# Optimization experiments

Measured on AMD Instinct MI355X. Metric: run time of the kernel, lower is better.

## Reference

```python
import jax, jax.numpy as jnp
import numpy as np

NUM_HEADS = 8
SCALE = 1.0
BN_EPS = 1e-5


def _mlp1d(x, W1, g1, b1, W2):
    # Conv1d(k=1, bias=False) -> BatchNorm1d (training-mode batch stats) -> ReLU -> Conv1d(k=1, bias=False)
    h = jnp.einsum('oi,bil->bol', W1, x)
    mu = h.mean(axis=(0, 2), keepdims=True)
    var = h.var(axis=(0, 2), keepdims=True)  # biased var, as torch BN training
    h = (h - mu) * jax.lax.rsqrt(var + BN_EPS)
    h = jax.nn.relu(h * g1[None, :, None] + b1[None, :, None])
    return jnp.einsum('oi,bil->bol', W2, h)


def setup_inputs() -> dict:
    key = jax.random.key(0)
    ks = jax.random.split(key, 8)
    b, c, hh, ww = 64, 2048, 14, 14
    hid, out = 4096, 256
    d = {'x': jax.random.normal(ks[0], (b, c, hh, ww), jnp.float32)}

    def w(k, o, i):
        return jax.random.normal(k, (o, i), jnp.float32) * np.float32(1.0 / np.sqrt(i))

    i = 1
    for pre in ('p', 'pp', 'po'):  # proj, proj_pixel, proj_obj
        d[pre + 'W1'] = w(ks[i], hid, c); i += 1
        d[pre + 'G1'] = jnp.ones((hid,), jnp.float32)
        d[pre + 'B1'] = jnp.zeros((hid,), jnp.float32)
        d[pre + 'W2'] = w(ks[i], out, hid); i += 1
    return d


def reference(x, pW1, pG1, pB1, pW2, ppW1, ppG1, ppB1, ppW2, poW1, poG1, poB1, poW2):
    b, c, h, w = x.shape
    xf = x.reshape(b, c, h * w)                      # flatten(2)
    x_pool = xf.mean(axis=2, keepdims=True)          # adaptive_avg_pool2d(x, 1)
    z_g = _mlp1d(x_pool, pW1, pG1, pB1, pW2)         # [b, 256, 1]
    z_feat = _mlp1d(xf, ppW1, ppG1, ppB1, ppW2)      # [b, 256, hw]
    # F.normalize(dim=1) with eps=1e-12, then /scale
    nrm = jnp.maximum(jnp.linalg.norm(z_feat, axis=1, keepdims=True), 1e-12)
    attn = (z_feat / nrm) / SCALE
    attn = attn.reshape(b, NUM_HEADS, -1, h * w)     # [b, nh, 256/nh, hw]
    attn = jax.nn.softmax(attn, axis=-1)
    x4 = xf.reshape(b, NUM_HEADS, c // NUM_HEADS, h * w)
    # torch.matmul(x, obj_attn.transpose(3, 2)) : [b,nh,c/nh,hw] @ [b,nh,hw,q]
    obj_val = jnp.einsum('bnkl,bnql->bnkq', x4, attn).reshape(b, c, -1)  # [b, c, 256/nh]
    obj_val = _mlp1d(obj_val, poW1, poG1, poB1, poW2)                    # [b, 256, 32]
    return z_g, obj_val
```

## Files before the change

kernel.cpp:

```cpp
#include <hip/hip_runtime.h>
#include <hip/hip_bf16.h>

using bf16 = __hip_bfloat16;
typedef __bf16 bf16x8v __attribute__((ext_vector_type(8)));
typedef float f32x4 __attribute__((ext_vector_type(4)));

#define BN_EPS 1e-5f

__device__ __forceinline__ float ldval(const float* p) { return *p; }
__device__ __forceinline__ float ldval(const bf16* p)  { return __bfloat162float(*p); }
__device__ __forceinline__ void stval(float* p, float v) { *p = v; }
__device__ __forceinline__ void stval(bf16* p, float v)  { *p = __float2bfloat16(v); }

__device__ __forceinline__ void gload_lds16(const void* g, void* l) {
    __builtin_amdgcn_global_load_lds(
        (const __attribute__((address_space(1))) unsigned int*)g,
        (__attribute__((address_space(3))) unsigned int*)l,
        16, 0, 0);
}

template<typename TC>
__global__ __launch_bounds__(512, 2) void mfma_tn8(
    const bf16* __restrict__ A, const bf16* __restrict__ B, TC* __restrict__ C,
    int M, int N, int K, float* __restrict__ ps, float* __restrict__ pq)
{
    __shared__ char lds[131072];
    const int NT = K >> 6;
    const int tid = threadIdx.x;
    const int lane = tid & 63;
    const int wv = tid >> 6;
    const int wm = wv >> 2;
    const int wn = wv & 3;

    const int nbx = gridDim.x;
    int flat = blockIdx.y * nbx + blockIdx.x;
    const int cpx = (nbx * gridDim.y) >> 3;
    flat = (flat & 7) * cpx + (flat >> 3);
    const int mtile = flat / nbx;
    const long m0 = (long)mtile * 256;
    const long n0 = (long)(flat % nbx) * 256;

    const int trow = tid >> 3;
    const int ks = (((tid & 7) ^ ((tid >> 3) & 7)) << 3);
    const bf16* Arow0 = A + (m0 + trow) * (long)K + ks;
    const bf16* Brow0 = B + (n0 + trow) * (long)K + ks;
    char* ldsA = (char*)lds + tid * 16;
    char* ldsB = (char*)lds + 32768 + tid * 16;

    auto stage_a = [&](int bbuf, int kt) {
        const bf16* g = Arow0 + ((long)kt << 6);
        char* d = ldsA + (bbuf << 16);
        gload_lds16(g, d);
        gload_lds16(g + ((long)K << 6),  d + 8192);
        gload_lds16(g + ((long)K << 7),  d + 16384);
        gload_lds16(g + 192L * (long)K,  d + 24576);
    };
    auto stage_b = [&](int bbuf, int kt) {
        const bf16* g = Brow0 + ((long)kt << 6);
        char* d = ldsB + (bbuf << 16);
        gload_lds16(g, d);
        gload_lds16(g + ((long)K << 6),  d + 8192);
        gload_lds16(g + ((long)K << 7),  d + 16384);
        gload_lds16(g + 192L * (long)K,  d + 24576);
    };

    const int fr = lane & 15, fc = lane >> 4;
    const int ca0 = ((fc ^ (fr & 7)) << 4);
    const int ca1 = (((4 + fc) ^ (fr & 7)) << 4);

    f32x4 acc[8][4];
#pragma unroll
    for (int m = 0; m < 8; ++m)
#pragma unroll
        for (int n = 0; n < 4; ++n) acc[m][n] = (f32x4){0.f, 0.f, 0.f, 0.f};

    stage_a(0, 0); stage_b(0, 0); stage_a(1, 1); stage_b(1, 1);

    for (int T = 0; T < NT; ++T) {
        const int bb = T & 1;
        const char* Ard = (const char*)lds + (bb << 16) + (wm * 128 + fr) * 128;
        const char* Brd = (const char*)lds + (bb << 16) + 32768 + (wn * 64 + fr) * 128;

        if (T == 0)          { asm volatile("s_waitcnt vmcnt(8)" ::: "memory"); }
        else if (T < NT - 1) { asm volatile("s_waitcnt vmcnt(4)" ::: "memory"); }
        else                 { asm volatile("s_waitcnt vmcnt(0)" ::: "memory"); }
        __builtin_amdgcn_s_barrier();
        __builtin_amdgcn_sched_barrier(0);

        bf16x8v a0[8], a1[8];
#pragma unroll
        for (int m = 0; m < 8; ++m) {
            a0[m] = *(const bf16x8v*)(Ard + m * 2048 + ca0);
            a1[m] = *(const bf16x8v*)(Ard + m * 2048 + ca1);
        }
        bf16x8v b00 = *(const bf16x8v*)(Brd + ca0);
        bf16x8v b01 = *(const bf16x8v*)(Brd + ca1);
        bf16x8v b10 = *(const bf16x8v*)(Brd + 2048 + ca0);
        bf16x8v b11 = *(const bf16x8v*)(Brd + 2048 + ca1);

        if (T >= 1 && T + 1 < NT) stage_b(bb ^ 1, T + 1);

        __builtin_amdgcn_s_setprio(1);
#pragma unroll
        for (int m = 0; m < 8; ++m) {
            acc[m][0] = __builtin_amdgcn_mfma_f32_16x16x32_bf16(a0[m], b00, acc[m][0], 0, 0, 0);
            acc[m][0] = __builtin_amdgcn_mfma_f32_16x16x32_bf16(a1[m], b01, acc[m][0], 0, 0, 0);
            acc[m][1] = __builtin_amdgcn_mfma_f32_16x16x32_bf16(a0[m], b10, acc[m][1], 0, 0, 0);
            acc[m][1] = __builtin_amdgcn_mfma_f32_16x16x32_bf16(a1[m], b11, acc[m][1], 0, 0, 0);
        }
        __builtin_amdgcn_s_setprio(0);

        __builtin_amdgcn_s_barrier();
        __builtin_amdgcn_sched_barrier(0);

        bf16x8v b20 = *(const bf16x8v*)(Brd + 2 * 2048 + ca0);
        bf16x8v b21 = *(const bf16x8v*)(Brd + 2 * 2048 + ca1);
        bf16x8v b30 = *(const bf16x8v*)(Brd + 3 * 2048 + ca0);
        bf16x8v b31 = *(const bf16x8v*)(Brd + 3 * 2048 + ca1);

        if (T + 2 < NT) stage_a(bb, T + 2);

        __builtin_amdgcn_s_setprio(1);
#pragma unroll
        for (int m = 0; m < 8; ++m) {
            acc[m][2] = __builtin_amdgcn_mfma_f32_16x16x32_bf16(a0[m], b20, acc[m][2], 0, 0, 0);
            acc[m][2] = __builtin_amdgcn_mfma_f32_16x16x32_bf16(a1[m], b21, acc[m][2], 0, 0, 0);
            acc[m][3] = __builtin_amdgcn_mfma_f32_16x16x32_bf16(a0[m], b30, acc[m][3], 0, 0, 0);
            acc[m][3] = __builtin_amdgcn_mfma_f32_16x16x32_bf16(a1[m], b31, acc[m][3], 0, 0, 0);
        }
        __builtin_amdgcn_s_setprio(0);
    }

#pragma unroll
    for (int m = 0; m < 8; ++m) {
        long gr = m0 + wm * 128 + m * 16 + fc * 4;
#pragma unroll
        for (int n = 0; n < 4; ++n) {
            long gc = n0 + wn * 64 + n * 16 + fr;
            TC* cp = C + gr * N + gc;
#pragma unroll
            for (int r = 0; r < 4; ++r) stval(cp + (long)r * N, acc[m][n][r]);
        }
    }

    if (ps != nullptr) {
        __syncthreads();
        float* red = (float*)lds;
        float cs[4], cq[4];
#pragma unroll
        for (int n = 0; n < 4; ++n) {
            float s = 0.f, q = 0.f;
#pragma unroll
            for (int m = 0; m < 8; ++m)
#pragma unroll
                for (int r = 0; r < 4; ++r) {
                    float v = __bfloat162float(__float2bfloat16(acc[m][n][r]));
                    s += v; q += v * v;
                }
            s += __shfl_xor(s, 16, 64); s += __shfl_xor(s, 32, 64);
            q += __shfl_xor(q, 16, 64); q += __shfl_xor(q, 32, 64);
            cs[n] = s; cq[n] = q;
        }
        if (fc == 0) {
#pragma unroll
            for (int n = 0; n < 4; ++n) {
                red[wv * 64 + n * 16 + fr] = cs[n];
                red[512 + wv * 64 + n * 16 + fr] = cq[n];
            }
        }
        __syncthreads();
        if (tid < 256) {
            int c = tid, wnn = c >> 6, idx = c & 63;
            float s = red[wnn * 64 + idx] + red[(4 + wnn) * 64 + idx];
            float q = red[512 + wnn * 64 + idx] + red[512 + (4 + wnn) * 64 + idx];
            ps[(long)mtile * N + n0 + c] = s;
            pq[(long)mtile * N + n0 + c] = q;
        }
    }
}

template<typename TC>
__global__ __launch_bounds__(256) void mfma_tn(
    const bf16* __restrict__ A, const bf16* __restrict__ B, TC* __restrict__ C,
    int M, int N, int K)
{
    __shared__ alignas(16) unsigned short As[128 * 32];
    __shared__ alignas(16) unsigned short Bs[128 * 32];

    const int tid = threadIdx.x;
    const int l = tid & 63;
    const long m0 = (long)blockIdx.y * 128;
    const long n0 = (long)blockIdx.x * 128;
    const int wr = (tid >> 7) & 1;
    const int wc = (tid >> 6) & 1;

    const int off0 = tid * 16;
    const int row0 = off0 >> 6;
    const int kp0  = (off0 >> 4) & 3;
    const bf16* Ag0 = A + (m0 + row0) * (long)K + kp0 * 8;
    const bf16* Ag1 = A + (m0 + row0 + 64) * (long)K + kp0 * 8;
    const bf16* Bg0 = B + (n0 + row0) * (long)K + kp0 * 8;
    const bf16* Bg1 = B + (n0 + row0 + 64) * (long)K + kp0 * 8;
    char* Asl0 = (char*)As + off0;
    char* Asl1 = (char*)As + off0 + 4096;
    char* Bsl0 = (char*)Bs + off0;
    char* Bsl1 = (char*)Bs + off0 + 4096;

    f32x4 acc[4][4];
#pragma unroll
    for (int m = 0; m < 4; ++m)
#pragma unroll
        for (int n = 0; n < 4; ++n) acc[m][n] = (f32x4){0.f, 0.f, 0.f, 0.f};

    const int fr = l & 15;
    const int fc = l >> 4;
    int aoff[4], boff[4];
#pragma unroll
    for (int m = 0; m < 4; ++m) aoff[m] = ((wr * 64 + m * 16 + fr) * 4 + fc) * 16;
#pragma unroll
    for (int n = 0; n < 4; ++n) boff[n] = ((wc * 64 + n * 16 + fr) * 4 + fc) * 16;

    for (int k0 = 0; k0 < K; k0 += 32) {
        gload_lds16(Ag0 + k0, Asl0);
        gload_lds16(Ag1 + k0, Asl1);
        gload_lds16(Bg0 + k0, Bsl0);
        gload_lds16(Bg1 + k0, Bsl1);
        __syncthreads();

        bf16x8v af[4], bfr[4];
#pragma unroll
        for (int m = 0; m < 4; ++m) af[m]  = *(const bf16x8v*)((const char*)As + aoff[m]);
#pragma unroll
        for (int n = 0; n < 4; ++n) bfr[n] = *(const bf16x8v*)((const char*)Bs + boff[n]);
#pragma unroll
        for (int m = 0; m < 4; ++m)
#pragma unroll
            for (int n = 0; n < 4; ++n)
                acc[m][n] = __builtin_amdgcn_mfma_f32_16x16x32_bf16(af[m], bfr[n], acc[m][n], 0, 0, 0);
        __syncthreads();
    }

#pragma unroll
    for (int m = 0; m < 4; ++m) {
        long gr = m0 + wr * 64 + m * 16 + fc * 4;
#pragma unroll
        for (int n = 0; n < 4; ++n) {
            long gc = n0 + wc * 64 + n * 16 + fr;
            TC* cp = C + gr * N + gc;
#pragma unroll
            for (int r = 0; r < 4; ++r) stval(cp + (long)r * N, acc[m][n][r]);
        }
    }
}

__global__ __launch_bounds__(256) void mfma_tn_bn(
    const bf16* __restrict__ A, const bf16* __restrict__ B, float* __restrict__ C,
    int M, int N, int K, const float* __restrict__ ta, const float* __restrict__ tc)
{
    __shared__ alignas(16) unsigned short As[128 * 32];
    __shared__ alignas(16) unsigned short Bs[128 * 32];

    const int tid = threadIdx.x;
    const int l = tid & 63;
    const long m0 = (long)blockIdx.y * 128;
    const long n0 = (long)blockIdx.x * 128;
    const int wr = (tid >> 7) & 1;
    const int wc = (tid >> 6) & 1;

    const int off0 = tid * 16;
    const int row0 = off0 >> 6;
    const int kp0  = (off0 >> 4) & 3;
    const bf16* Ag0 = A + (m0 + row0) * (long)K + kp0 * 8;
    const bf16* Ag1 = A + (m0 + row0 + 64) * (long)K + kp0 * 8;
    const bf16* Bg0 = B + (n0 + row0) * (long)K + kp0 * 8;
    const bf16* Bg1 = B + (n0 + row0 + 64) * (long)K + kp0 * 8;
    char* Asl0 = (char*)As + off0;
    char* Asl1 = (char*)As + off0 + 4096;
    char* Bsl0 = (char*)Bs + off0;
    char* Bsl1 = (char*)Bs + off0 + 4096;

    f32x4 acc[4][4];
#pragma unroll
    for (int m = 0; m < 4; ++m)
#pragma unroll
        for (int n = 0; n < 4; ++n) acc[m][n] = (f32x4){0.f, 0.f, 0.f, 0.f};

    const int fr = l & 15;
    const int fc = l >> 4;
    int aoff[4], boff[4];
#pragma unroll
    for (int m = 0; m < 4; ++m) aoff[m] = ((wr * 64 + m * 16 + fr) * 4 + fc) * 16;
#pragma unroll
    for (int n = 0; n < 4; ++n) boff[n] = ((wc * 64 + n * 16 + fr) * 4 + fc) * 16;

    for (int k0 = 0; k0 < K; k0 += 32) {
        gload_lds16(Bg0 + k0, Bsl0);
        gload_lds16(Bg1 + k0, Bsl1);

        union { bf16 h[8]; uint4 u; } r0, r1;
        r0.u = *(const uint4*)(Ag0 + k0);
        r1.u = *(const uint4*)(Ag1 + k0);
        const int kb = k0 + kp0 * 8;
        float4 av0 = *(const float4*)(ta + kb);
        float4 av1 = *(const float4*)(ta + kb + 4);
        float4 cv0 = *(const float4*)(tc + kb);
        float4 cv1 = *(const float4*)(tc + kb + 4);
        float av[8] = {av0.x, av0.y, av0.z, av0.w, av1.x, av1.y, av1.z, av1.w};
        float cv[8] = {cv0.x, cv0.y, cv0.z, cv0.w, cv1.x, cv1.y, cv1.z, cv1.w};
#pragma unroll
        for (int j = 0; j < 8; ++j) {
            float v = fmaxf(fmaf(av[j], __bfloat162float(r0.h[j]), cv[j]), 0.f);
            r0.h[j] = __float2bfloat16(v);
            v = fmaxf(fmaf(av[j], __bfloat162float(r1.h[j]), cv[j]), 0.f);
            r1.h[j] = __float2bfloat16(v);
        }
        *(uint4*)Asl0 = r0.u;
        *(uint4*)Asl1 = r1.u;
        __syncthreads();

        bf16x8v af[4], bfr[4];
#pragma unroll
        for (int m = 0; m < 4; ++m) af[m]  = *(const bf16x8v*)((const char*)As + aoff[m]);
#pragma unroll
        for (int n = 0; n < 4; ++n) bfr[n] = *(const bf16x8v*)((const char*)Bs + boff[n]);
#pragma unroll
        for (int m = 0; m < 4; ++m)
#pragma unroll
            for (int n = 0; n < 4; ++n)
                acc[m][n] = __builtin_amdgcn_mfma_f32_16x16x32_bf16(af[m], bfr[n], acc[m][n], 0, 0, 0);
        __syncthreads();
    }

#pragma unroll
    for (int m = 0; m < 4; ++m) {
        long gr = m0 + wr * 64 + m * 16 + fc * 4;
#pragma unroll
        for (int n = 0; n < 4; ++n) {
            long gc = n0 + wc * 64 + n * 16 + fr;
            float* cp = C + gr * N + gc;
#pragma unroll
            for (int r = 0; r < 4; ++r) cp[(long)r * N] = acc[m][n][r];
        }
    }
}

__global__ __launch_bounds__(256) void mfma_tn_sk(
    const bf16* __restrict__ A, const bf16* __restrict__ B, float* __restrict__ Cp,
    int M, int N, int K, int KCH)
{
    __shared__ alignas(16) unsigned short As[128 * 32];
    __shared__ alignas(16) unsigned short Bs[128 * 32];

    const int tid = threadIdx.x;
    const int l = tid & 63;
    const long m0 = (long)blockIdx.y * 128;
    const long n0 = (long)blockIdx.x * 128;
    const int wr = (tid >> 7) & 1;
    const int wc = (tid >> 6) & 1;
    const int ksrt = blockIdx.z * KCH;

    const int off0 = tid * 16;
    const int row0 = off0 >> 6;
    const int kp0  = (off0 >> 4) & 3;
    const bf16* Ag0 = A + (m0 + row0) * (long)K + kp0 * 8 + ksrt;
    const bf16* Ag1 = A + (m0 + row0 + 64) * (long)K + kp0 * 8 + ksrt;
    const bf16* Bg0 = B + (n0 + row0) * (long)K + kp0 * 8 + ksrt;
    const bf16* Bg1 = B + (n0 + row0 + 64) * (long)K + kp0 * 8 + ksrt;
    char* Asl0 = (char*)As + off0;
    char* Asl1 = (char*)As + off0 + 4096;
    char* Bsl0 = (char*)Bs + off0;
    char* Bsl1 = (char*)Bs + off0 + 4096;

    f32x4 acc[4][4];
#pragma unroll
    for (int m = 0; m < 4; ++m)
#pragma unroll
        for (int n = 0; n < 4; ++n) acc[m][n] = (f32x4){0.f, 0.f, 0.f, 0.f};

    const int fr = l & 15;
    const int fc = l >> 4;
    int aoff[4], boff[4];
#pragma unroll
    for (int m = 0; m < 4; ++m) aoff[m] = ((wr * 64 + m * 16 + fr) * 4 + fc) * 16;
#pragma unroll
    for (int n = 0; n < 4; ++n) boff[n] = ((wc * 64 + n * 16 + fr) * 4 + fc) * 16;

    for (int k0 = 0; k0 < KCH; k0 += 32) {
        gload_lds16(Ag0 + k0, Asl0);
        gload_lds16(Ag1 + k0, Asl1);
        gload_lds16(Bg0 + k0, Bsl0);
        gload_lds16(Bg1 + k0, Bsl1);
        __syncthreads();

        bf16x8v af[4], bfr[4];
#pragma unroll
        for (int m = 0; m < 4; ++m) af[m]  = *(const bf16x8v*)((const char*)As + aoff[m]);
#pragma unroll
        for (int n = 0; n < 4; ++n) bfr[n] = *(const bf16x8v*)((const char*)Bs + boff[n]);
#pragma unroll
        for (int m = 0; m < 4; ++m)
#pragma unroll
            for (int n = 0; n < 4; ++n)
                acc[m][n] = __builtin_amdgcn_mfma_f32_16x16x32_bf16(af[m], bfr[n], acc[m][n], 0, 0, 0);
        __syncthreads();
    }

    float* Cb = Cp + (long)blockIdx.z * M * N;
#pragma unroll
    for (int m = 0; m < 4; ++m) {
        long gr = m0 + wr * 64 + m * 16 + fc * 4;
#pragma unroll
        for (int n = 0; n < 4; ++n) {
            long gc = n0 + wc * 64 + n * 16 + fr;
            float* cp = Cb + gr * N + gc;
#pragma unroll
            for (int r = 0; r < 4; ++r) cp[(long)r * N] = acc[m][n][r];
        }
    }
}

__global__ __launch_bounds__(256) void objmm_k(
    const bf16* __restrict__ attnP, const bf16* __restrict__ xP, bf16* __restrict__ objinT)
{
    __shared__ alignas(16) unsigned short As[32 * 32];
    __shared__ alignas(16) unsigned short Bs[256 * 32];
    const int tid = threadIdx.x, lane = tid & 63, wv = tid >> 6;
    const int b = blockIdx.x >> 3, h = blockIdx.x & 7;
    const bf16* Ab = attnP + ((long)(b * 256 + h * 32)) * 224;
    const bf16* Bb = xP + ((long)(b * 2048 + h * 256)) * 224;
    const int fr = lane & 15, fc = lane >> 4;
    const int srow = tid >> 2, schk = tid & 3;

    f32x4 acc[2][4];
#pragma unroll
    for (int m = 0; m < 2; ++m)
#pragma unroll
        for (int n = 0; n < 4; ++n) acc[m][n] = (f32x4){0.f, 0.f, 0.f, 0.f};

    for (int k0 = 0; k0 < 224; k0 += 32) {
        if (wv < 2)
            gload_lds16(Ab + (long)srow * 224 + schk * 8 + k0, (char*)As + tid * 16);
#pragma unroll
        for (int j = 0; j < 4; ++j)
            gload_lds16(Bb + (long)(j * 64 + srow) * 224 + schk * 8 + k0,
                        (char*)Bs + j * 4096 + tid * 16);
        __syncthreads();

        bf16x8v af[2], bfr[4];
#pragma unroll
        for (int m = 0; m < 2; ++m)
            af[m] = *(const bf16x8v*)((const char*)As + (m * 16 + fr) * 64 + fc * 16);
#pragma unroll
        for (int n = 0; n < 4; ++n)
            bfr[n] = *(const bf16x8v*)((const char*)Bs + (wv * 64 + n * 16 + fr) * 64 + fc * 16);
#pragma unroll
        for (int m = 0; m < 2; ++m)
#pragma unroll
            for (int n = 0; n < 4; ++n)
                acc[m][n] = __builtin_amdgcn_mfma_f32_16x16x32_bf16(af[m], bfr[n], acc[m][n], 0, 0, 0);
        __syncthreads();
    }

#pragma unroll
    for (int m = 0; m < 2; ++m) {
        long gr = (long)b * 32 + m * 16 + fc * 4;
#pragma unroll
        for (int n = 0; n < 4; ++n) {
            long gc = (long)h * 256 + wv * 64 + n * 16 + fr;
            bf16* cp = objinT + gr * 2048 + gc;
#pragma unroll
            for (int r = 0; r < 4; ++r) cp[(long)r * 2048] = __float2bfloat16(acc[m][n][r]);
        }
    }
}

__global__ __launch_bounds__(256) void foldout_k(const float* __restrict__ p, float* __restrict__ out)
{
    int o = blockIdx.x * 256 + threadIdx.x;
    int b = o >> 13, rem = o & 8191, q = rem >> 5, tt = rem & 31;
    long base = ((long)(b * 32 + tt)) * 256 + q;
    float s = p[base] + p[524288 + base] + p[2 * 524288 + base] + p[3 * 524288 + base];
    out[o] = s;
}

__global__ __launch_bounds__(256) void tobf16_k(const float* __restrict__ in, bf16* __restrict__ out, long n)
{
    long i = ((long)blockIdx.x * 256 + threadIdx.x) * 8;
    if (i >= n) return;
    float4 v0 = *(const float4*)(in + i);
    float4 v1 = *(const float4*)(in + i + 4);
    union { bf16 h[8]; uint4 u; } r;
    r.h[0] = __float2bfloat16(v0.x); r.h[1] = __float2bfloat16(v0.y);
    r.h[2] = __float2bfloat16(v0.z); r.h[3] = __float2bfloat16(v0.w);
    r.h[4] = __float2bfloat16(v1.x); r.h[5] = __float2bfloat16(v1.y);
    r.h[6] = __float2bfloat16(v1.z); r.h[7] = __float2bfloat16(v1.w);
    *(uint4*)(out + i) = r.u;
}

__global__ __launch_bounds__(256) void packx2_k(const float* __restrict__ x,
    bf16* __restrict__ XT, bf16* __restrict__ xP, float* __restrict__ xpT)
{
    __shared__ unsigned short tile[196 * 66 + 4];
    __shared__ float pp[64];
    const int t = threadIdx.x;
    const int b = blockIdx.y, c0 = blockIdx.x * 64;
    const int wvi = t >> 6, lane = t & 63;

    for (int p = 0; p < 16; ++p) {
        int c = p * 4 + wvi;
        const float* row = x + ((long)b * 2048 + c0 + c) * 196;
        float v0 = row[lane];
        float v1 = row[lane + 64];
        float v2 = row[lane + 128];
        float v3 = (lane < 4) ? row[lane + 192] : 0.f;
        bf16 h0 = __float2bfloat16(v0);
        bf16 h1 = __float2bfloat16(v1);
        bf16 h2 = __float2bfloat16(v2);
        bf16 h3 = __float2bfloat16(v3);
        tile[lane * 66 + c]         = *(unsigned short*)&h0;
        tile[(lane + 64) * 66 + c]  = *(unsigned short*)&h1;
        tile[(lane + 128) * 66 + c] = *(unsigned short*)&h2;
        if (lane < 4) tile[(lane + 192) * 66 + c] = *(unsigned short*)&h3;
        bf16* xr = xP + ((long)b * 2048 + c0 + c) * 224;
        xr[lane] = h0; xr[lane + 64] = h1; xr[lane + 128] = h2;
        int l3 = lane + 192;
        if (lane < 4) xr[l3] = h3;
        else if (l3 < 224) xr[l3] = __float2bfloat16(0.f);
        float s = v0 + v1 + v2 + v3;
#pragma unroll
        for (int off = 32; off; off >>= 1) s += __shfl_xor(s, off, 64);
        if (lane == 0) pp[c] = s;
    }
    __syncthreads();
    if (t < 64) xpT[(c0 + t) * 64 + b] = pp[t] * (1.f / 196.f);

    for (int u = t; u < 196 * 8; u += 256) {
        int l = u >> 3, cc = u & 7;
        const unsigned short* sp = &tile[l * 66 + cc * 8];
        uint4 r;
        r.x = *(const unsigned int*)(sp);
        r.y = *(const unsigned int*)(sp + 2);
        r.z = *(const unsigned int*)(sp + 4);
        r.w = *(const unsigned int*)(sp + 6);
        *(uint4*)(&XT[((long)b * 196 + l) * 2048 + c0 + cc * 8]) = r;
    }
}

__global__ __launch_bounds__(256) void colstat1_k(const bf16* __restrict__ H,
    float* __restrict__ ps, float* __restrict__ pq)
{
    int c  = blockIdx.x * 256 + threadIdx.x;
    int r0 = blockIdx.y * 256;
    float s = 0.f, q = 0.f;
    for (int r = r0; r < r0 + 256; ++r) {
        float v = __bfloat162float(H[(long)r * 4096 + c]);
        s += v; q += v * v;
    }
    ps[(long)blockIdx.y * 4096 + c] = s;
    pq[(long)blockIdx.y * 4096 + c] = q;
}

__global__ __launch_bounds__(256) void colstat2_k(const float* __restrict__ ps, const float* __restrict__ pq,
    int P, float invN, const float* __restrict__ g, const float* __restrict__ be,
    float* __restrict__ ta, float* __restrict__ tc)
{
    int c = blockIdx.x * 256 + threadIdx.x;
    float s = 0.f, q = 0.f;
    for (int p = 0; p < P; ++p) { s += ps[(long)p * 4096 + c]; q += pq[(long)p * 4096 + c]; }
    float mu  = s * invN;
    float var = q * invN - mu * mu;
    float a   = g[c] * rsqrtf(var + BN_EPS);
    ta[c] = a;
    tc[c] = be[c] - mu * a;
}

__global__ __launch_bounds__(256) void bnrelu_k(bf16* __restrict__ H,
    const float* __restrict__ ta, const float* __restrict__ tc, long n8)
{
    long i = (long)blockIdx.x * 256 + threadIdx.x;
    if (i >= n8) return;
    long base = i * 8;
    int  c0   = (int)(base & 4095);
    union { bf16 h[8]; uint4 u; } r;
    r.u = *(uint4*)(H + base);
#pragma unroll
    for (int j = 0; j < 8; ++j) {
        float v = __bfloat162float(r.h[j]);
        v = fmaxf(ta[c0 + j] * v + tc[c0 + j], 0.f);
        r.h[j] = __float2bfloat16(v);
    }
    *(uint4*)(H + base) = r.u;
}

__global__ __launch_bounds__(256) void norm2_k(const float* __restrict__ z, float* __restrict__ invn, int J)
{
    int j = blockIdx.x * 4 + (threadIdx.x >> 6);
    int l = threadIdx.x & 63;
    if (j >= J) return;
    const float* row = z + (long)j * 256;
    float s = 0.f;
#pragma unroll
    for (int i = 0; i < 4; ++i) { float v = row[l + 64 * i]; s += v * v; }
#pragma unroll
    for (int off = 32; off; off >>= 1) s += __shfl_xor(s, off, 64);
    if (l == 0) invn[j] = 1.f / fmaxf(sqrtf(s), 1e-12f);
}

__global__ __launch_bounds__(256) void softmax2_k(const float* __restrict__ z,
    const float* __restrict__ invn, bf16* __restrict__ attnP)
{
    int row  = blockIdx.x * 4 + (threadIdx.x >> 6);
    int lane = threadIdx.x & 63;
    int b = row >> 8, q = row & 255;
    float v[4];
    float mx = -INFINITY;
#pragma unroll
    for (int i = 0; i < 4; ++i) {
        int l = lane + 64 * i;
        if (l < 196) {
            int j = b * 196 + l;
            v[i] = z[(long)j * 256 + q] * invn[j];
        } else v[i] = -INFINITY;
        mx = fmaxf(mx, v[i]);
    }
#pragma unroll
    for (int off = 32; off; off >>= 1) mx = fmaxf(mx, __shfl_xor(mx, off, 64));
    float s = 0.f;
#pragma unroll
    for (int i = 0; i < 4; ++i) {
        v[i] = (lane + 64 * i < 196) ? __expf(v[i] - mx) : 0.f;
        s += v[i];
    }
#pragma unroll
    for (int off = 32; off; off >>= 1) s += __shfl_xor(s, off, 64);
    float is = 1.f / s;
    bf16* rp = attnP + (long)row * 224;
#pragma unroll
    for (int i = 0; i < 4; ++i) {
        int l = lane + 64 * i;
        if (l < 196) rp[l] = __float2bfloat16(v[i] * is);
        else if (l < 224) rp[l] = __float2bfloat16(0.f);
    }
}

template<bool TRANS>
__global__ __launch_bounds__(256) void gemmsk_k(
    const float* __restrict__ A, const float* __restrict__ B, float* __restrict__ Cp,
    int M, int N, int K, int lda, int ldbk, int KCH,
    const float* __restrict__ tra, const float* __restrict__ trc)
{
    constexpr int BM = 64, BN = 64, BK = 16;
    __shared__ float As[BK][BM + 4];
    __shared__ float Bs[BK][BN + 4];

    const int tid = threadIdx.x;
    const int m0 = blockIdx.y * BM;
    const int ks = blockIdx.z * KCH;
    const int ke = min(K, ks + KCH);

    const int tIdm = tid / 16;
    const int tIdn = tid % 16;
    const int aK  = tid % BK;
    const int aM0 = tid / BK;
    const int bN  = tid % BN;
    const int bK0 = tid / BN;

    float acc[4][4];
#pragma unroll
    for (int u = 0; u < 4; ++u)
#pragma unroll
        for (int v = 0; v < 4; ++v) acc[u][v] = 0.f;

    for (int k0 = ks; k0 < ke; k0 += BK) {
#pragma unroll
        for (int i = 0; i < 4; ++i) {
            int m = aM0 + 16 * i;
            int gk = k0 + aK, gm = m0 + m;
            float v = 0.f;
            if (gk < ke && gm < M) v = A[(long)gm * lda + gk];
            As[aK][m] = v;
        }
#pragma unroll
        for (int i = 0; i < 4; ++i) {
            int kk = bK0 + 4 * i;
            int gk = k0 + kk;
            float v = 0.f;
            if (gk < ke && bN < N) {
                v = B[(long)gk * ldbk + bN];
                if (TRANS) v = fmaxf(tra[gk] * v + trc[gk], 0.f);
            }
            Bs[kk][bN] = v;
        }
        __syncthreads();
#pragma unroll
        for (int kk = 0; kk < BK; ++kk) {
            float a[4], b[4];
#pragma unroll
            for (int u = 0; u < 4; ++u) a[u] = As[kk][tIdm * 4 + u];
#pragma unroll
            for (int v = 0; v < 4; ++v) b[v] = Bs[kk][tIdn * 4 + v];
#pragma unroll
            for (int u = 0; u < 4; ++u)
#pragma unroll
                for (int v = 0; v < 4; ++v)
                    acc[u][v] = fmaf(a[u], b[v], acc[u][v]);
        }
        __syncthreads();
    }

    float* Cb = Cp + (long)blockIdx.z * M * N;
#pragma unroll
    for (int u = 0; u < 4; ++u) {
        int gm = m0 + tIdm * 4 + u;
        if (gm >= M) continue;
#pragma unroll
        for (int v = 0; v < 4; ++v) {
            int gn = tIdn * 4 + v;
            if (gn < N) Cb[(long)gm * N + gn] = acc[u][v];
        }
    }
}

__global__ __launch_bounds__(256) void skreduce_k(const float* __restrict__ Cp, int P, long MN,
    int Nn, int ldm, int ldn, float* __restrict__ out)
{
    long i = (long)blockIdx.x * 256 + threadIdx.x;
    if (i >= MN) return;
    float s = 0.f;
    for (int p = 0; p < P; ++p) s += Cp[(long)p * MN + i];
    int m = (int)(i / Nn), n = (int)(i % Nn);
    out[(long)m * ldm + (long)n * ldn] = s;
}

__global__ __launch_bounds__(256) void bnstat_k(const float* __restrict__ H, int L,
    const float* __restrict__ g, const float* __restrict__ be,
    float* __restrict__ ta, float* __restrict__ tc, float invN)
{
    int o = blockIdx.x;
    int tid = threadIdx.x;
    float s = 0.f, s2 = 0.f;
    for (int i = tid; i < L; i += 256) {
        float v = H[(long)o * L + i];
        s += v; s2 += v * v;
    }
    for (int off = 32; off; off >>= 1) {
        s  += __shfl_down(s, off, 64);
        s2 += __shfl_down(s2, off, 64);
    }
    __shared__ float rs[4], rs2[4];
    int wv = tid >> 6, ln = tid & 63;
    if (ln == 0) { rs[wv] = s; rs2[wv] = s2; }
    __syncthreads();
    if (tid == 0) {
        float S = 0.f, S2 = 0.f;
        for (int w = 0; w < 4; ++w) { S += rs[w]; S2 += rs2[w]; }
        float mu  = S * invN;
        float var = S2 * invN - mu * mu;
        float a   = g[o] * rsqrtf(var + BN_EPS);
        ta[o] = a;
        tc[o] = be[o] - mu * a;
    }
}

extern "C" void kernel_launch(void* const* d_in, const int* in_sizes, int n_in,
                              void* d_out, int out_size, void* d_ws, size_t ws_size,
                              hipStream_t stream)
{
    const float* x    = (const float*)d_in[0];
    const float* pW1  = (const float*)d_in[1];
    const float* pG1  = (const float*)d_in[2];
    const float* pB1  = (const float*)d_in[3];
    const float* pW2  = (const float*)d_in[4];
    const float* ppW1 = (const float*)d_in[5];
    const float* ppG1 = (const float*)d_in[6];
    const float* ppB1 = (const float*)d_in[7];
    const float* ppW2 = (const float*)d_in[8];
    const float* poW1 = (const float*)d_in[9];
    const float* poG1 = (const float*)d_in[10];
    const float* poB1 = (const float*)d_in[11];
    const float* poW2 = (const float*)d_in[12];
    float* out = (float*)d_out;
    (void)in_sizes; (void)n_in; (void)out_size; (void)ws_size;

    char* w = (char*)d_ws;
    auto alloc = [&](size_t bytes) -> char* {
        char* p = w; w += (bytes + 255) & ~(size_t)255; return p;
    };
    bf16* ppW1b = (bf16*)alloc((size_t)4096 * 2048 * 2);
    bf16* ppW2b = (bf16*)alloc((size_t)256 * 4096 * 2);
    bf16* poW1b = (bf16*)alloc((size_t)4096 * 2048 * 2);
    bf16* poW2b = (bf16*)alloc((size_t)256 * 4096 * 2);
    char* region1 = alloc((size_t)12544 * 2048 * 2);
    bf16*  XT     = (bf16*)region1;
    bf16*  attnP  = (bf16*)region1;
    bf16*  objinT = (bf16*)(region1 + 12845056);
    bf16*  hobjT  = (bf16*)(region1 + 12845056 + 8388608);
    bf16* xP     = (bf16*)alloc((size_t)64 * 2048 * 224 * 2);
    bf16* hfeatT = (bf16*)alloc((size_t)12544 * 4096 * 2);
    float* zfeatT = (float*)alloc((size_t)12544 * 256 * 4);
    float* ps    = (float*)alloc((size_t)49 * 4096 * 4);
    float* pq    = (float*)alloc((size_t)49 * 4096 * 4);
    float* invn  = (float*)alloc((size_t)12544 * 4);
    float* a2    = (float*)alloc(4096 * 4);
    float* c2    = (float*)alloc(4096 * 4);
    float* a3    = (float*)alloc(4096 * 4);
    float* c3    = (float*)alloc(4096 * 4);
    float* xpT   = (float*)alloc((size_t)2048 * 64 * 4);
    float* h1    = (float*)alloc((size_t)4096 * 64 * 4);
    float* a1    = (float*)alloc(4096 * 4);
    float* c1    = (float*)alloc(4096 * 4);
    float* skp1  = (float*)alloc((size_t)16 * 4096 * 64 * 4);
    float* skp2  = (float*)alloc((size_t)32 * 256 * 64 * 4);
    float* skp5  = (float*)alloc((size_t)4 * 2048 * 256 * 4);

    tobf16_k<<<4096, 256, 0, stream>>>(ppW1, ppW1b, (long)4096 * 2048);
    tobf16_k<<<512,  256, 0, stream>>>(ppW2, ppW2b, (long)256 * 4096);
    tobf16_k<<<4096, 256, 0, stream>>>(poW1, poW1b, (long)4096 * 2048);
    tobf16_k<<<512,  256, 0, stream>>>(poW2, poW2b, (long)256 * 4096);
    packx2_k<<<dim3(32, 64), 256, 0, stream>>>(x, XT, xP, xpT);

    gemmsk_k<false><<<dim3(1, 64, 16), 256, 0, stream>>>(
        pW1, xpT, skp1, 4096, 64, 2048, 2048, 64, 128, nullptr, nullptr);
    skreduce_k<<<1024, 256, 0, stream>>>(skp1, 16, (long)4096 * 64, 64, 64, 1, h1);
    bnstat_k<<<4096, 256, 0, stream>>>(h1, 64, pG1, pB1, a1, c1, 1.f / 64.f);
    gemmsk_k<true><<<dim3(1, 4, 32), 256, 0, stream>>>(
        pW2, h1, skp2, 256, 64, 4096, 4096, 64, 128, a1, c1);
    skreduce_k<<<64, 256, 0, stream>>>(skp2, 32, (long)256 * 64, 64, 1, 256, out);

    mfma_tn8<bf16><<<dim3(16, 49), 512, 0, stream>>>(XT, ppW1b, hfeatT, 12544, 4096, 2048, ps, pq);
    colstat2_k<<<16, 256, 0, stream>>>(ps, pq, 49, 1.f / 12544.f, ppG1, ppB1, a2, c2);

    mfma_tn_bn<<<dim3(2, 98), 256, 0, stream>>>(hfeatT, ppW2b, zfeatT, 12544, 256, 4096, a2, c2);

    norm2_k<<<3136, 256, 0, stream>>>(zfeatT, invn, 12544);
    softmax2_k<<<4096, 256, 0, stream>>>(zfeatT, invn, attnP);

    objmm_k<<<512, 256, 0, stream>>>(attnP, xP, objinT);

    mfma_tn<bf16><<<dim3(32, 16), 256, 0, stream>>>(objinT, poW1b, hobjT, 2048, 4096, 2048);

    colstat1_k<<<dim3(16, 8), 256, 0, stream>>>(hobjT, ps, pq);
    colstat2_k<<<16, 256, 0, stream>>>(ps, pq, 8, 1.f / 2048.f, poG1, poB1, a3, c3);
    bnrelu_k<<<4096, 256, 0, stream>>>(hobjT, a3, c3, (long)2048 * 4096 / 8);

    mfma_tn_sk<<<dim3(2, 16, 4), 256, 0, stream>>>(hobjT, poW2b, skp5, 2048, 256, 4096, 1024);
    foldout_k<<<2048, 256, 0, stream>>>(skp5, out + 16384);
}
```

Before: 708.2 us.

## Fuse BN statistics and BN-ReLU into GEMMs, merge conversions and reductions

New measurement: 688.7 us. -2.7%, faster.

```diff
diff --git a/kernel.cpp b/kernel.cpp
--- a/kernel.cpp
+++ b/kernel.cpp
@@ -7,8 +7,6 @@
 
 #define BN_EPS 1e-5f
 
-__device__ __forceinline__ float ldval(const float* p) { return *p; }
-__device__ __forceinline__ float ldval(const bf16* p)  { return __bfloat162float(*p); }
 __device__ __forceinline__ void stval(float* p, float v) { *p = v; }
 __device__ __forceinline__ void stval(bf16* p, float v)  { *p = __float2bfloat16(v); }
 
@@ -182,7 +180,7 @@
 template<typename TC>
 __global__ __launch_bounds__(256) void mfma_tn(
     const bf16* __restrict__ A, const bf16* __restrict__ B, TC* __restrict__ C,
-    int M, int N, int K)
+    int M, int N, int K, float* __restrict__ ps, float* __restrict__ pq)
 {
     __shared__ alignas(16) unsigned short As[128 * 32];
     __shared__ alignas(16) unsigned short Bs[128 * 32];
@@ -251,6 +249,40 @@
             for (int r = 0; r < 4; ++r) stval(cp + (long)r * N, acc[m][n][r]);
         }
     }
+
+    if (ps != nullptr) {
+        float* red = (float*)As;
+        float cs[4], cq[4];
+#pragma unroll
+        for (int n = 0; n < 4; ++n) {
+            float s = 0.f, q = 0.f;
+#pragma unroll
+            for (int m = 0; m < 4; ++m)
+#pragma unroll
+                for (int r = 0; r < 4; ++r) {
+                    float v = __bfloat162float(__float2bfloat16(acc[m][n][r]));
+                    s += v; q += v * v;
+                }
+            s += __shfl_xor(s, 16, 64); s += __shfl_xor(s, 32, 64);
+            q += __shfl_xor(q, 16, 64); q += __shfl_xor(q, 32, 64);
+            cs[n] = s; cq[n] = q;
+        }
+        if (fc == 0) {
+#pragma unroll
+            for (int n = 0; n < 4; ++n) {
+                int c = wc * 64 + n * 16 + fr;
+                red[wr * 128 + c] = cs[n];
+                red[256 + wr * 128 + c] = cq[n];
+            }
+        }
+        __syncthreads();
+        if (tid < 128) {
+            float s = red[tid] + red[128 + tid];
+            float q = red[256 + tid] + red[384 + tid];
+            ps[(long)blockIdx.y * N + n0 + tid] = s;
+            pq[(long)blockIdx.y * N + n0 + tid] = q;
+        }
+    }
 }
 
 __global__ __launch_bounds__(256) void mfma_tn_bn(
@@ -344,9 +376,9 @@
     }
 }
 
-__global__ __launch_bounds__(256) void mfma_tn_sk(
+__global__ __launch_bounds__(256) void mfma_tn_skbn(
     const bf16* __restrict__ A, const bf16* __restrict__ B, float* __restrict__ Cp,
-    int M, int N, int K, int KCH)
+    int M, int N, int K, int KCH, const float* __restrict__ ta, const float* __restrict__ tc)
 {
     __shared__ alignas(16) unsigned short As[128 * 32];
     __shared__ alignas(16) unsigned short Bs[128 * 32];
@@ -386,10 +418,28 @@
     for (int n = 0; n < 4; ++n) boff[n] = ((wc * 64 + n * 16 + fr) * 4 + fc) * 16;
 
     for (int k0 = 0; k0 < KCH; k0 += 32) {
-        gload_lds16(Ag0 + k0, Asl0);
-        gload_lds16(Ag1 + k0, Asl1);
         gload_lds16(Bg0 + k0, Bsl0);
         gload_lds16(Bg1 + k0, Bsl1);
+
+        union { bf16 h[8]; uint4 u; } r0, r1;
+        r0.u = *(const uint4*)(Ag0 + k0);
+        r1.u = *(const uint4*)(Ag1 + k0);
+        const int kb = ksrt + k0 + kp0 * 8;
+        float4 av0 = *(const float4*)(ta + kb);
+        float4 av1 = *(const float4*)(ta + kb + 4);
+        float4 cv0 = *(const float4*)(tc + kb);
+        float4 cv1 = *(const float4*)(tc + kb + 4);
+        float av[8] = {av0.x, av0.y, av0.z, av0.w, av1.x, av1.y, av1.z, av1.w};
+        float cv[8] = {cv0.x, cv0.y, cv0.z, cv0.w, cv1.x, cv1.y, cv1.z, cv1.w};
+#pragma unroll
+        for (int j = 0; j < 8; ++j) {
+            float v = fmaxf(fmaf(av[j], __bfloat162float(r0.h[j]), cv[j]), 0.f);
+            r0.h[j] = __float2bfloat16(v);
+            v = fmaxf(fmaf(av[j], __bfloat162float(r1.h[j]), cv[j]), 0.f);
+            r1.h[j] = __float2bfloat16(v);
+        }
+        *(uint4*)Asl0 = r0.u;
+        *(uint4*)Asl1 = r1.u;
         __syncthreads();
 
         bf16x8v af[4], bfr[4];
@@ -483,18 +533,28 @@
     out[o] = s;
 }
 
-__global__ __launch_bounds__(256) void tobf16_k(const float* __restrict__ in, bf16* __restrict__ out, long n)
-{
+__global__ __launch_bounds__(256) void convert4_k(
+    const float* __restrict__ w1, const float* __restrict__ w2,
+    const float* __restrict__ w3, const float* __restrict__ w4,
+    bf16* __restrict__ o1, bf16* __restrict__ o2,
+    bf16* __restrict__ o3, bf16* __restrict__ o4)
+{
+    const long L1 = 8388608, L2 = 1048576;
     long i = ((long)blockIdx.x * 256 + threadIdx.x) * 8;
-    if (i >= n) return;
-    float4 v0 = *(const float4*)(in + i);
-    float4 v1 = *(const float4*)(in + i + 4);
+    const float* src; bf16* dst; long e;
+    if (i < L1)                { src = w1; dst = o1; e = i; }
+    else if (i < L1 + L2)      { src = w2; dst = o2; e = i - L1; }
+    else if (i < 2*L1 + L2)    { src = w3; dst = o3; e = i - L1 - L2; }
+    else if (i < 2*L1 + 2*L2)  { src = w4; dst = o4; e = i - 2*L1 - L2; }
+    else return;
+    float4 v0 = *(const float4*)(src + e);
+    float4 v1 = *(const float4*)(src + e + 4);
     union { bf16 h[8]; uint4 u; } r;
     r.h[0] = __float2bfloat16(v0.x); r.h[1] = __float2bfloat16(v0.y);
     r.h[2] = __float2bfloat16(v0.z); r.h[3] = __float2bfloat16(v0.w);
     r.h[4] = __float2bfloat16(v1.x); r.h[5] = __float2bfloat16(v1.y);
     r.h[6] = __float2bfloat16(v1.z); r.h[7] = __float2bfloat16(v1.w);
-    *(uint4*)(out + i) = r.u;
+    *(uint4*)(dst + e) = r.u;
 }
 
 __global__ __launch_bounds__(256) void packx2_k(const float* __restrict__ x,
@@ -521,11 +581,6 @@
         tile[(lane + 64) * 66 + c]  = *(unsigned short*)&h1;
         tile[(lane + 128) * 66 + c] = *(unsigned short*)&h2;
         if (lane < 4) tile[(lane + 192) * 66 + c] = *(unsigned short*)&h3;
-        bf16* xr = xP + ((long)b * 2048 + c0 + c) * 224;
-        xr[lane] = h0; xr[lane + 64] = h1; xr[lane + 128] = h2;
-        int l3 = lane + 192;
-        if (lane < 4) xr[l3] = h3;
-        else if (l3 < 224) xr[l3] = __float2bfloat16(0.f);
         float s = v0 + v1 + v2 + v3;
 #pragma unroll
         for (int off = 32; off; off >>= 1) s += __shfl_xor(s, off, 64);
@@ -544,20 +599,18 @@
         r.w = *(const unsigned int*)(sp + 6);
         *(uint4*)(&XT[((long)b * 196 + l) * 2048 + c0 + cc * 8]) = r;
     }
-}
-
-__global__ __launch_bounds__(256) void colstat1_k(const bf16* __restrict__ H,
-    float* __restrict__ ps, float* __restrict__ pq)
-{
-    int c  = blockIdx.x * 256 + threadIdx.x;
-    int r0 = blockIdx.y * 256;
-    float s = 0.f, q = 0.f;
-    for (int r = r0; r < r0 + 256; ++r) {
-        float v = __bfloat162float(H[(long)r * 4096 + c]);
-        s += v; q += v * v;
-    }
-    ps[(long)blockIdx.y * 4096 + c] = s;
-    pq[(long)blockIdx.y * 4096 + c] = q;
+
+    for (int u = t; u < 64 * 28; u += 256) {
+        int c = u / 28, ch = u % 28;
+        int l0 = ch * 8;
+        union { unsigned short h[8]; uint4 v; } r;
+#pragma unroll
+        for (int e = 0; e < 8; ++e) {
+            int ll = l0 + e;
+            r.h[e] = (ll < 196) ? tile[ll * 66 + c] : (unsigned short)0;
+        }
+        *(uint4*)(xP + ((long)b * 2048 + c0 + c) * 224 + l0) = r.v;
+    }
 }
 
 __global__ __launch_bounds__(256) void colstat2_k(const float* __restrict__ ps, const float* __restrict__ pq,
@@ -572,24 +625,6 @@
     float a   = g[c] * rsqrtf(var + BN_EPS);
     ta[c] = a;
     tc[c] = be[c] - mu * a;
-}
-
-__global__ __launch_bounds__(256) void bnrelu_k(bf16* __restrict__ H,
-    const float* __restrict__ ta, const float* __restrict__ tc, long n8)
-{
-    long i = (long)blockIdx.x * 256 + threadIdx.x;
-    if (i >= n8) return;
-    long base = i * 8;
-    int  c0   = (int)(base & 4095);
-    union { bf16 h[8]; uint4 u; } r;
-    r.u = *(uint4*)(H + base);
-#pragma unroll
-    for (int j = 0; j < 8; ++j) {
-        float v = __bfloat162float(r.h[j]);
-        v = fmaxf(ta[c0 + j] * v + tc[c0 + j], 0.f);
-        r.h[j] = __float2bfloat16(v);
-    }
-    *(uint4*)(H + base) = r.u;
 }
 
 __global__ __launch_bounds__(256) void norm2_k(const float* __restrict__ z, float* __restrict__ invn, int J)
@@ -721,6 +756,31 @@
     }
 }
 
+__global__ __launch_bounds__(256) void skbn_k(const float* __restrict__ Cp,
+    const float* __restrict__ g, const float* __restrict__ be,
+    float* __restrict__ h1, float* __restrict__ ta, float* __restrict__ tc)
+{
+    int o = blockIdx.x * 4 + (threadIdx.x >> 6);
+    int b = threadIdx.x & 63;
+    float s = 0.f;
+#pragma unroll
+    for (int p = 0; p < 16; ++p) s += Cp[(long)p * 262144 + o * 64 + b];
+    h1[o * 64 + b] = s;
+    float s1 = s, s2 = s * s;
+#pragma unroll
+    for (int off = 32; off; off >>= 1) {
+        s1 += __shfl_down(s1, off, 64);
+        s2 += __shfl_down(s2, off, 64);
+    }
+    if (b == 0) {
+        float mu  = s1 * (1.f / 64.f);
+        float var = s2 * (1.f / 64.f) - mu * mu;
+        float a   = g[o] * rsqrtf(var + BN_EPS);
+        ta[o] = a;
+        tc[o] = be[o] - mu * a;
+    }
+}
+
 __global__ __launch_bounds__(256) void skreduce_k(const float* __restrict__ Cp, int P, long MN,
     int Nn, int ldm, int ldn, float* __restrict__ out)
 {
@@ -730,36 +790,6 @@
     for (int p = 0; p < P; ++p) s += Cp[(long)p * MN + i];
     int m = (int)(i / Nn), n = (int)(i % Nn);
     out[(long)m * ldm + (long)n * ldn] = s;
-}
-
-__global__ __launch_bounds__(256) void bnstat_k(const float* __restrict__ H, int L,
-    const float* __restrict__ g, const float* __restrict__ be,
-    float* __restrict__ ta, float* __restrict__ tc, float invN)
-{
-    int o = blockIdx.x;
-    int tid = threadIdx.x;
-    float s = 0.f, s2 = 0.f;
-    for (int i = tid; i < L; i += 256) {
-        float v = H[(long)o * L + i];
-        s += v; s2 += v * v;
-    }
-    for (int off = 32; off; off >>= 1) {
-        s  += __shfl_down(s, off, 64);
-        s2 += __shfl_down(s2, off, 64);
-    }
-    __shared__ float rs[4], rs2[4];
-    int wv = tid >> 6, ln = tid & 63;
-    if (ln == 0) { rs[wv] = s; rs2[wv] = s2; }
-    __syncthreads();
-    if (tid == 0) {
-        float S = 0.f, S2 = 0.f;
-        for (int w = 0; w < 4; ++w) { S += rs[w]; S2 += rs2[w]; }
-        float mu  = S * invN;
-        float var = S2 * invN - mu * mu;
-        float a   = g[o] * rsqrtf(var + BN_EPS);
-        ta[o] = a;
-        tc[o] = be[o] - mu * a;
-    }
 }
 
 extern "C" void kernel_launch(void* const* d_in, const int* in_sizes, int n_in,
@@ -813,16 +843,12 @@
     float* skp2  = (float*)alloc((size_t)32 * 256 * 64 * 4);
     float* skp5  = (float*)alloc((size_t)4 * 2048 * 256 * 4);
 
-    tobf16_k<<<4096, 256, 0, stream>>>(ppW1, ppW1b, (long)4096 * 2048);
-    tobf16_k<<<512,  256, 0, stream>>>(ppW2, ppW2b, (long)256 * 4096);
-    tobf16_k<<<4096, 256, 0, stream>>>(poW1, poW1b, (long)4096 * 2048);
-    tobf16_k<<<512,  256, 0, stream>>>(poW2, poW2b, (long)256 * 4096);
+    convert4_k<<<9216, 256, 0, stream>>>(ppW1, ppW2, poW1, poW2, ppW1b, ppW2b, poW1b, poW2b);
     packx2_k<<<dim3(32, 64), 256, 0, stream>>>(x, XT, xP, xpT);
 
     gemmsk_k<false><<<dim3(1, 64, 16), 256, 0, stream>>>(
         pW1, xpT, skp1, 4096, 64, 2048, 2048, 64, 128, nullptr, nullptr);
-    skreduce_k<<<1024, 256, 0, stream>>>(skp1, 16, (long)4096 * 64, 64, 64, 1, h1);
-    bnstat_k<<<4096, 256, 0, stream>>>(h1, 64, pG1, pB1, a1, c1, 1.f / 64.f);
+    skbn_k<<<1024, 256, 0, stream>>>(skp1, pG1, pB1, h1, a1, c1);
     gemmsk_k<true><<<dim3(1, 4, 32), 256, 0, stream>>>(
         pW2, h1, skp2, 256, 64, 4096, 4096, 64, 128, a1, c1);
     skreduce_k<<<64, 256, 0, stream>>>(skp2, 32, (long)256 * 64, 64, 1, 256, out);
@@ -837,12 +863,9 @@
 
     objmm_k<<<512, 256, 0, stream>>>(attnP, xP, objinT);
 
-    mfma_tn<bf16><<<dim3(32, 16), 256, 0, stream>>>(objinT, poW1b, hobjT, 2048, 4096, 2048);
-
-    colstat1_k<<<dim3(16, 8), 256, 0, stream>>>(hobjT, ps, pq);
-    colstat2_k<<<16, 256, 0, stream>>>(ps, pq, 8, 1.f / 2048.f, poG1, poB1, a3, c3);
-    bnrelu_k<<<4096, 256, 0, stream>>>(hobjT, a3, c3, (long)2048 * 4096 / 8);
-
-    mfma_tn_sk<<<dim3(2, 16, 4), 256, 0, stream>>>(hobjT, poW2b, skp5, 2048, 256, 4096, 1024);
+    mfma_tn<bf16><<<dim3(32, 16), 256, 0, stream>>>(objinT, poW1b, hobjT, 2048, 4096, 2048, ps, pq);
+    colstat2_k<<<16, 256, 0, stream>>>(ps, pq, 16, 1.f / 2048.f, poG1, poB1, a3, c3);
+
+    mfma_tn_skbn<<<dim3(2, 16, 4), 256, 0, stream>>>(hobjT, poW2b, skp5, 2048, 256, 4096, 1024, a3, c3);
     foldout_k<<<2048, 256, 0, stream>>>(skp5, out + 16384);
 }
```
